# Performance work log

Measured on AMD Instinct MI355X. Metric: run time of the kernel, lower is better.

Reference implementation:

```python
import jax, jax.numpy as jnp
import numpy as np

N = 100000
E = 1600000
G = 128


def _degrees(src, dst, n):
    ones = jnp.ones(src.shape[0], dtype=jnp.float32)
    deg_out = jax.ops.segment_sum(ones, src, num_segments=n)
    deg_in = jax.ops.segment_sum(ones, dst, num_segments=n)
    return jnp.maximum(deg_out, 1.0), jnp.maximum(deg_in, 1.0)


def gcn_conv(x, W, b, src, dst, norm_out, norm_in):
    # DGL GraphConv, norm='both': scale src by d_out^-1/2, sum over edges,
    # scale dst by d_in^-1/2, then linear. Weight applied first (out<=in) --
    # mathematically identical, cheaper gather.
    h = (x * norm_out[:, None]) @ W          # [N, out]
    m = h[src]                               # [E, out] gather
    agg = jax.ops.segment_sum(m, dst, num_segments=N)  # [N, out] scatter-add
    return agg * norm_in[:, None] + b


def setup_inputs() -> dict:
    key = jax.random.key(0)
    ks = jax.random.split(key, 8)
    x = jax.random.normal(ks[0], (N, 128), dtype=jnp.float32)
    W1 = jax.random.normal(ks[1], (128, 64), dtype=jnp.float32) * (1.0 / np.sqrt(128))
    b1 = jnp.zeros((64,), dtype=jnp.float32)
    W2 = jax.random.normal(ks[2], (64, 16), dtype=jnp.float32) * (1.0 / np.sqrt(64))
    b2 = jnp.zeros((16,), dtype=jnp.float32)
    src = jax.random.randint(ks[3], (E,), 0, N, dtype=jnp.int32)
    dst = jax.random.randint(ks[4], (E,), 0, N, dtype=jnp.int32)
    graph_ids = jnp.sort(jax.random.randint(ks[5], (N,), 0, G, dtype=jnp.int32))
    return {"x": x, "W1": W1, "b1": b1, "W2": W2, "b2": b2,
            "src": src, "dst": dst, "graph_ids": graph_ids}


def reference(x, W1, b1, W2, b2, src, dst, graph_ids):
    deg_out, deg_in = _degrees(src, dst, N)
    norm_out = jax.lax.rsqrt(deg_out)
    norm_in = jax.lax.rsqrt(deg_in)
    h = gcn_conv(x, W1, b1, src, dst, norm_out, norm_in)
    h = jax.nn.relu(h)
    # dropout(p=0.2) is identity in eval mode
    h = gcn_conv(h, W2, b2, src, dst, norm_out, norm_in)
    # dgl.mean_nodes: per-graph mean pooling
    sums = jax.ops.segment_sum(h, graph_ids, num_segments=G)      # [G, 16]
    counts = jax.ops.segment_sum(jnp.ones((N,), jnp.float32), graph_ids, num_segments=G)
    return sums / jnp.maximum(counts, 1.0)[:, None]
```

## Files before the change

kernel.cpp:

```cpp
#include <hip/hip_runtime.h>
#include <hip/hip_fp16.h>

#define N_NODES 100000
#define N_EDGES 1600000
#define N_GRAPHS 128
#define SB 391
#define CAP 4608
#define NBLK 512
#define NE4 (N_EDGES / 4)
#define CH4 782
#define LDX 136

typedef unsigned long long u64;
typedef unsigned int u32;
typedef unsigned char u8;
typedef _Float16 f16;
typedef f16 half8 __attribute__((ext_vector_type(8)));
typedef f16 half4v __attribute__((ext_vector_type(4)));
typedef float floatx4 __attribute__((ext_vector_type(4)));

__global__ void k_init(int* __restrict__ cur_d, int* __restrict__ cur_s) {
  int t = blockIdx.x * blockDim.x + threadIdx.x;
  if (t < SB) { cur_d[t] = t * CAP; cur_s[t] = t * CAP; }
}

__global__ __launch_bounds__(256) void k_fuse(const int4* __restrict__ src4,
                                              const int4* __restrict__ dst4,
                                              int* __restrict__ cur_d,
                                              int* __restrict__ cur_s,
                                              u32* __restrict__ ed,
                                              u8* __restrict__ ssk8) {
  __shared__ int hd[SB], hs[SB], ld[SB], ls[SB];
  const int t = threadIdx.x, b = blockIdx.x;
  for (int j = t; j < SB; j += 256) { hd[j] = 0; hs[j] = 0; }
  __syncthreads();
  const int start = b * CH4, end = min(start + CH4, NE4);
  for (int i = start + t; i < end; i += 256) {
    int4 d = dst4[i]; int4 s = src4[i];
    atomicAdd(&hd[d.x >> 8], 1); atomicAdd(&hd[d.y >> 8], 1);
    atomicAdd(&hd[d.z >> 8], 1); atomicAdd(&hd[d.w >> 8], 1);
    atomicAdd(&hs[s.x >> 8], 1); atomicAdd(&hs[s.y >> 8], 1);
    atomicAdd(&hs[s.z >> 8], 1); atomicAdd(&hs[s.w >> 8], 1);
  }
  __syncthreads();
  for (int j = t; j < SB; j += 256) {
    ld[j] = atomicAdd(&cur_d[j], hd[j]);
    ls[j] = atomicAdd(&cur_s[j], hs[j]);
  }
  __syncthreads();
  for (int i = start + t; i < end; i += 256) {
    int4 d4 = dst4[i]; int4 s4 = src4[i];
    {
      int d = d4.x, s = s4.x;
      int pd = atomicAdd(&ld[d >> 8], 1);
      ed[pd] = ((u32)(d & 255) << 24) | (u32)s;
      int ps = atomicAdd(&ls[s >> 8], 1);
      ssk8[ps] = (u8)(s & 255);
    }
    {
      int d = d4.y, s = s4.y;
      int pd = atomicAdd(&ld[d >> 8], 1);
      ed[pd] = ((u32)(d & 255) << 24) | (u32)s;
      int ps = atomicAdd(&ls[s >> 8], 1);
      ssk8[ps] = (u8)(s & 255);
    }
    {
      int d = d4.z, s = s4.z;
      int pd = atomicAdd(&ld[d >> 8], 1);
      ed[pd] = ((u32)(d & 255) << 24) | (u32)s;
      int ps = atomicAdd(&ls[s >> 8], 1);
      ssk8[ps] = (u8)(s & 255);
    }
    {
      int d = d4.w, s = s4.w;
      int pd = atomicAdd(&ld[d >> 8], 1);
      ed[pd] = ((u32)(d & 255) << 24) | (u32)s;
      int ps = atomicAdd(&ls[s >> 8], 1);
      ssk8[ps] = (u8)(s & 255);
    }
  }
}

__global__ __launch_bounds__(256) void k_bucket_csr(const u32* __restrict__ ed,
                                                    const u8* __restrict__ ssk8,
                                                    const int* __restrict__ cur_d,
                                                    const int* __restrict__ cur_s,
                                                    int* __restrict__ row_ptr,
                                                    int* __restrict__ deg,
                                                    float* __restrict__ norm_in,
                                                    float* __restrict__ norm_out,
                                                    int* __restrict__ edge_src) {
  __shared__ int hist[256], scanbuf[256], cursor[256], hist2[256];
  const int b = blockIdx.x, t = threadIdx.x;
  const int base = b << 8;
  const int lo = b * CAP;
  const int hiD = cur_d[b];
  const int hiS = cur_s[b];
  hist[t] = 0; hist2[t] = 0;
  __syncthreads();
  for (int i = lo + t; i < hiS; i += 256) atomicAdd(&hist2[ssk8[i]], 1);
  for (int i = lo + t; i < hiD; i += 256) atomicAdd(&hist[ed[i] >> 24], 1);
  __syncthreads();
  int node = base + t;
  if (node < N_NODES)
    norm_out[node] = rsqrtf(fmaxf((float)hist2[t], 1.0f));
  int v = hist[t];
  scanbuf[t] = v;
  __syncthreads();
  for (int off = 1; off < 256; off <<= 1) {
    int a = (t >= off) ? scanbuf[t - off] : 0;
    __syncthreads(); scanbuf[t] += a; __syncthreads();
  }
  int excl = scanbuf[t] - v;
  if (node < N_NODES) {
    row_ptr[node] = lo + excl;
    deg[node] = v;
    norm_in[node] = rsqrtf(fmaxf((float)v, 1.0f));
  }
  cursor[t] = excl;
  __syncthreads();
  for (int i = lo + t; i < hiD; i += 256) {
    u32 e = ed[i];
    int p = atomicAdd(&cursor[e >> 24], 1);
    edge_src[lo + p] = (int)(e & 0x00FFFFFFu);
  }
}

__global__ __launch_bounds__(256) void k_gemm1(const float* __restrict__ x,
                                               const float* __restrict__ W1,
                                               const float* __restrict__ norm_out,
                                               __half* __restrict__ h1h) {
  __shared__ __align__(16) f16 Xs[64 * LDX];
  __shared__ __align__(16) f16 Ws[64 * LDX];
  const int t = threadIdx.x;
  const int row0 = blockIdx.x * 64;

  const float4* W4 = (const float4*)W1;
  for (int i = t; i < 2048; i += 256) {
    int k = i >> 4, n4 = (i & 15) * 4;
    float4 v = W4[i];
    Ws[(n4 + 0) * LDX + k] = (f16)v.x;
    Ws[(n4 + 1) * LDX + k] = (f16)v.y;
    Ws[(n4 + 2) * LDX + k] = (f16)v.z;
    Ws[(n4 + 3) * LDX + k] = (f16)v.w;
  }
  const float4* x4 = (const float4*)x;
  #pragma unroll
  for (int i = 0; i < 8; ++i) {
    int idx = t + 256 * i;
    int r = idx >> 5, c4 = idx & 31;
    int row = row0 + r;
    float4 v = make_float4(0.f, 0.f, 0.f, 0.f);
    if (row < N_NODES) {
      float s = norm_out[row];
      v = x4[(size_t)row * 32 + c4];
      v.x *= s; v.y *= s; v.z *= s; v.w *= s;
    }
    half4v h = { (f16)v.x, (f16)v.y, (f16)v.z, (f16)v.w };
    *(half4v*)&Xs[r * LDX + c4 * 4] = h;
  }
  __syncthreads();

  const int w = t >> 6, l = t & 63;
  const int m = l & 15, quad = l >> 4;
  floatx4 c0 = {0.f,0.f,0.f,0.f}, c1 = {0.f,0.f,0.f,0.f};
  floatx4 c2 = {0.f,0.f,0.f,0.f}, c3 = {0.f,0.f,0.f,0.f};
  const f16* xrow = &Xs[(w * 16 + m) * LDX + quad * 8];
  const f16* wrow = &Ws[m * LDX + quad * 8];
  #pragma unroll
  for (int kb = 0; kb < 4; ++kb) {
    half8 a  = *(const half8*)(xrow + kb * 32);
    half8 b0 = *(const half8*)(wrow + kb * 32);
    half8 b1 = *(const half8*)(wrow + 16 * LDX + kb * 32);
    half8 b2 = *(const half8*)(wrow + 32 * LDX + kb * 32);
    half8 b3 = *(const half8*)(wrow + 48 * LDX + kb * 32);
    c0 = __builtin_amdgcn_mfma_f32_16x16x32_f16(a, b0, c0, 0, 0, 0);
    c1 = __builtin_amdgcn_mfma_f32_16x16x32_f16(a, b1, c1, 0, 0, 0);
    c2 = __builtin_amdgcn_mfma_f32_16x16x32_f16(a, b2, c2, 0, 0, 0);
    c3 = __builtin_amdgcn_mfma_f32_16x16x32_f16(a, b3, c3, 0, 0, 0);
  }
  #pragma unroll
  for (int r = 0; r < 4; ++r) {
    int row = row0 + w * 16 + quad * 4 + r;
    if (row < N_NODES + 1) {
      __half* dst = h1h + (size_t)row * 64 + m;
      dst[0]  = __float2half(c0[r]);
      dst[16] = __float2half(c1[r]);
      dst[32] = __float2half(c2[r]);
      dst[48] = __float2half(c3[r]);
    }
  }
}

__global__ __launch_bounds__(256) void k_gather_l1(const int* __restrict__ row_ptr,
                                                   const int* __restrict__ deg,
                                                   const int* __restrict__ edge_src,
                                                   const __half* __restrict__ h1h,
                                                   const float* __restrict__ norm_in,
                                                   const float* __restrict__ norm_out,
                                                   const float* __restrict__ b1,
                                                   const float* __restrict__ W2,
                                                   __half* __restrict__ h2h) {
  __shared__ __align__(16) f16 Ws2[16 * 72];
  __shared__ __align__(16) f16 Rs[4][16 * 72];
  const int t = threadIdx.x;
  for (int i = t; i < 1024; i += 256) {
    int k = i >> 4, n = i & 15;
    Ws2[n * 72 + k] = (f16)W2[i];
  }
  if (blockIdx.x == 0 && t < 16) h2h[(size_t)N_NODES * 16 + t] = __float2half(0.f);
  __syncthreads();

  const int w = t >> 6, l = t & 63;
  const int base = blockIdx.x * 64 + w * 16;
  if (base >= N_NODES) return;

  const int m = l & 15, q4 = l >> 4;
  const int node_l = min(base + m, N_NODES - 1);
  const int my_lo = row_ptr[node_l];
  const u32 my_deg = (u32)deg[node_l];
  const int lo_blk = __shfl(my_lo, 0, 64);
  const int hi_blk = __shfl(my_lo + (int)my_deg, 15, 64);

  const int s1e = 8 * (m >> 2) + (m & 3);
  const int s2e = s1e + 4;

  union U4 { u32 u[4]; half8 h; uint4 v; };

  U4 ib0, ib1;
  #pragma unroll
  for (int wj = 0; wj < 4; ++wj) {
    int k0 = q4 * 8 + 2 * wj, k1 = k0 + 1;
    ib0.u[wj] = (k0 == m      ? 0x3C00u : 0u) | (k1 == m      ? 0x3C000000u : 0u);
    ib1.u[wj] = (k0 == m + 16 ? 0x3C00u : 0u) | (k1 == m + 16 ? 0x3C000000u : 0u);
  }

  const uint4* __restrict__ h1u4 = (const uint4*)h1h;
  floatx4 acc0 = {0.f,0.f,0.f,0.f}, acc1 = {0.f,0.f,0.f,0.f};
  floatx4 acc2 = {0.f,0.f,0.f,0.f}, acc3 = {0.f,0.f,0.f,0.f};
  const floatx4 zf = {0.f,0.f,0.f,0.f};

  uint4 pa0, pa1, pb0, pb1;
  #define LOADC(CB) do {                                                      \
    int i1 = (CB) + s1e, i2 = (CB) + s2e;                                     \
    int sv1 = (i1 < hi_blk) ? edge_src[i1] : (int)N_NODES;                    \
    int sv2 = (i2 < hi_blk) ? edge_src[i2] : (int)N_NODES;                    \
    size_t r1 = (size_t)(u32)sv1 * 8u, r2 = (size_t)(u32)sv2 * 8u;            \
    pa0 = h1u4[r1 + (u32)q4];       pa1 = h1u4[r1 + 4u + (u32)q4];            \
    pb0 = h1u4[r2 + (u32)q4];       pb1 = h1u4[r2 + 4u + (u32)q4];            \
  } while (0)

  if (lo_blk < hi_blk) LOADC(lo_blk);
  #pragma unroll 1
  for (int cb = lo_blk; cb < hi_blk; cb += 32) {
    U4 ca0, ca1, cbb0, cbb1;
    ca0.v = pa0; ca1.v = pa1; cbb0.v = pb0; cbb1.v = pb1;
    if (cb + 32 < hi_blk) LOADC(cb + 32);

    u32 e0 = (u32)(cb - my_lo) + (u32)(q4 * 8);
    U4 s;
    s.u[0] = ((e0+0u)<my_deg?0x3C00u:0u) | ((e0+1u)<my_deg?0x3C000000u:0u);
    s.u[1] = ((e0+2u)<my_deg?0x3C00u:0u) | ((e0+3u)<my_deg?0x3C000000u:0u);
    s.u[2] = ((e0+4u)<my_deg?0x3C00u:0u) | ((e0+5u)<my_deg?0x3C000000u:0u);
    s.u[3] = ((e0+6u)<my_deg?0x3C00u:0u) | ((e0+7u)<my_deg?0x3C000000u:0u);

    {
      floatx4 o10 = __builtin_amdgcn_mfma_f32_16x16x32_f16(ca0.h,  ib0.h, zf, 0, 0, 0);
      floatx4 o11 = __builtin_amdgcn_mfma_f32_16x16x32_f16(ca0.h,  ib1.h, zf, 0, 0, 0);
      floatx4 o20 = __builtin_amdgcn_mfma_f32_16x16x32_f16(cbb0.h, ib0.h, zf, 0, 0, 0);
      floatx4 o21 = __builtin_amdgcn_mfma_f32_16x16x32_f16(cbb0.h, ib1.h, zf, 0, 0, 0);
      half8 bf0 = { (f16)o10[0], (f16)o10[1], (f16)o10[2], (f16)o10[3],
                    (f16)o20[0], (f16)o20[1], (f16)o20[2], (f16)o20[3] };
      half8 bf1 = { (f16)o11[0], (f16)o11[1], (f16)o11[2], (f16)o11[3],
                    (f16)o21[0], (f16)o21[1], (f16)o21[2], (f16)o21[3] };
      acc0 = __builtin_amdgcn_mfma_f32_16x16x32_f16(s.h, bf0, acc0, 0, 0, 0);
      acc1 = __builtin_amdgcn_mfma_f32_16x16x32_f16(s.h, bf1, acc1, 0, 0, 0);
    }
    {
      floatx4 o10 = __builtin_amdgcn_mfma_f32_16x16x32_f16(ca1.h,  ib0.h, zf, 0, 0, 0);
      floatx4 o11 = __builtin_amdgcn_mfma_f32_16x16x32_f16(ca1.h,  ib1.h, zf, 0, 0, 0);
      floatx4 o20 = __builtin_amdgcn_mfma_f32_16x16x32_f16(cbb1.h, ib0.h, zf, 0, 0, 0);
      floatx4 o21 = __builtin_amdgcn_mfma_f32_16x16x32_f16(cbb1.h, ib1.h, zf, 0, 0, 0);
      half8 bf0 = { (f16)o10[0], (f16)o10[1], (f16)o10[2], (f16)o10[3],
                    (f16)o20[0], (f16)o20[1], (f16)o20[2], (f16)o20[3] };
      half8 bf1 = { (f16)o11[0], (f16)o11[1], (f16)o11[2], (f16)o11[3],
                    (f16)o21[0], (f16)o21[1], (f16)o21[2], (f16)o21[3] };
      acc2 = __builtin_amdgcn_mfma_f32_16x16x32_f16(s.h, bf0, acc2, 0, 0, 0);
      acc3 = __builtin_amdgcn_mfma_f32_16x16x32_f16(s.h, bf1, acc3, 0, 0, 0);
    }
  }
  #undef LOADC

  const float bg0 = b1[m], bg1 = b1[16 + m], bg2 = b1[32 + m], bg3 = b1[48 + m];
  f16* Rw = &Rs[w][0];
  #pragma unroll
  for (int r = 0; r < 4; ++r) {
    int row = base + q4 * 4 + r;
    float ni = (row < N_NODES) ? norm_in[row] : 0.f;
    f16* dst = &Rw[(q4 * 4 + r) * 72 + m];
    dst[0]  = (f16)fmaxf(acc0[r] * ni + bg0, 0.f);
    dst[16] = (f16)fmaxf(acc1[r] * ni + bg1, 0.f);
    dst[32] = (f16)fmaxf(acc2[r] * ni + bg2, 0.f);
    dst[48] = (f16)fmaxf(acc3[r] * ni + bg3, 0.f);
  }
  asm volatile("s_waitcnt lgkmcnt(0)" ::: "memory");
  __builtin_amdgcn_sched_barrier(0);

  const f16* ra = &Rw[m * 72 + q4 * 8];
  const f16* rb = &Ws2[m * 72 + q4 * 8];
  half8 a0 = *(const half8*)ra;
  half8 a1 = *(const half8*)(ra + 32);
  half8 wb0 = *(const half8*)rb;
  half8 wb1 = *(const half8*)(rb + 32);
  floatx4 cc = {0.f,0.f,0.f,0.f};
  cc = __builtin_amdgcn_mfma_f32_16x16x32_f16(a0, wb0, cc, 0, 0, 0);
  cc = __builtin_amdgcn_mfma_f32_16x16x32_f16(a1, wb1, cc, 0, 0, 0);
  #pragma unroll
  for (int r = 0; r < 4; ++r) {
    int row = base + q4 * 4 + r;
    if (row < N_NODES)
      h2h[(size_t)row * 16 + m] = __float2half(cc[r] * norm_out[row]);
  }
}

__global__ __launch_bounds__(256) void k_gather_l2(const int* __restrict__ row_ptr,
                                                   const int* __restrict__ deg,
                                                   const int* __restrict__ edge_src,
                                                   const __half* __restrict__ h2h,
                                                   const float* __restrict__ norm_in,
                                                   float* __restrict__ agg2) {
  const int t = threadIdx.x;
  const int w = t >> 6;
  const int l = t & 63;
  const int n = blockIdx.x * 4 + w;
  const int f2 = l & 7;
  const int p = l >> 3;

  const u32* __restrict__ h2u = (const u32*)h2h;
  const int lo = row_ptr[n], hi = lo + deg[n];

  float ax = 0.f, ay = 0.f, bx = 0.f, by = 0.f;
  for (int base = lo; base < hi; base += 16) {
    int i1 = base + p, i2 = base + p + 8;
    int s0 = (i1 < hi) ? edge_src[i1] : (int)N_NODES;
    int s1 = (i2 < hi) ? edge_src[i2] : (int)N_NODES;
    u32 v0 = h2u[(u32)s0 * 8u + (u32)f2];
    u32 v1 = h2u[(u32)s1 * 8u + (u32)f2];
    float2 g0 = __half22float2(*(__half2*)&v0);
    float2 g1 = __half22float2(*(__half2*)&v1);
    ax += g0.x; ay += g0.y;
    bx += g1.x; by += g1.y;
  }
  float sx = ax + bx, sy = ay + by;
  sx += __shfl_xor(sx, 8, 64);  sy += __shfl_xor(sy, 8, 64);
  sx += __shfl_xor(sx, 16, 64); sy += __shfl_xor(sy, 16, 64);
  sx += __shfl_xor(sx, 32, 64); sy += __shfl_xor(sy, 32, 64);
  if (l < 8) {
    float ni = norm_in[n];
    ((float2*)agg2)[(size_t)n * 8 + f2] = make_float2(sx * ni, sy * ni);
  }
}

__global__ __launch_bounds__(256) void k_pool(const float* __restrict__ agg2,
                                              const float* __restrict__ b2,
                                              const int* __restrict__ gid,
                                              float* __restrict__ out) {
  const int g = blockIdx.x;
  __shared__ int s_lo, s_hi;
  if (threadIdx.x == 0) {
    int a = 0, b = N_NODES;
    while (a < b) { int m = (a + b) >> 1; if (gid[m] < g) a = m + 1; else b = m; }
    s_lo = a;
    b = N_NODES;
    while (a < b) { int m = (a + b) >> 1; if (gid[m] < g + 1) a = m + 1; else b = m; }
    s_hi = a;
  }
  __syncthreads();
  const int lo = s_lo, hi = s_hi, cnt = hi - lo;
  const int j = threadIdx.x & 15;
  const int r = threadIdx.x >> 4;
  float acc = 0.f;
  for (int n = lo + r; n < hi; n += 16)
    acc += agg2[(size_t)n * 16 + j];

  __shared__ float red[256];
  red[threadIdx.x] = acc;
  __syncthreads();
  #pragma unroll
  for (int s = 8; s > 0; s >>= 1) {
    if (r < s) red[threadIdx.x] += red[threadIdx.x + s * 16];
    __syncthreads();
  }
  if (r == 0)
    out[g * 16 + j] = (cnt > 0) ? (red[j] / (float)cnt + b2[j]) : 0.0f;
}

extern "C" void kernel_launch(void* const* d_in, const int* in_sizes, int n_in,
                              void* d_out, int out_size, void* d_ws, size_t ws_size,
                              hipStream_t stream) {
  const float* x   = (const float*)d_in[0];
  const float* W1  = (const float*)d_in[1];
  const float* b1  = (const float*)d_in[2];
  const float* W2  = (const float*)d_in[3];
  const float* b2  = (const float*)d_in[4];
  const int*   src = (const int*)d_in[5];
  const int*   dst = (const int*)d_in[6];
  const int*   gid = (const int*)d_in[7];
  float* out = (float*)d_out;

  int* wsi = (int*)d_ws;
  float* wsf = (float*)d_ws;

  float* norm_out = wsf + 0;
  float* norm_in  = wsf + 100000;
  int*   row_ptr  = wsi + 200000;
  int*   deg      = wsi + 300000;
  int*   cur_d    = wsi + 400000;
  int*   cur_s    = wsi + 400400;
  int*   edge_src = wsi + 400800;
  const size_t S  = 2202528;
  u8*    ssk8     = (u8*)(wsi + S);
  u32*   ed       = (u32*)(wsi + S + 450432);
  __half* h1h     = (__half*)(wsi + S);
  __half* h2h     = (__half*)(wsi + S + 3200032);
  float*  agg2    = (float*)(wsi + S);

  const int4* src4 = (const int4*)src;
  const int4* dst4 = (const int4*)dst;

  k_init      <<<2, 256, 0, stream>>>(cur_d, cur_s);
  k_fuse      <<<NBLK, 256, 0, stream>>>(src4, dst4, cur_d, cur_s, ed, ssk8);
  k_bucket_csr<<<SB, 256, 0, stream>>>(ed, ssk8, cur_d, cur_s, row_ptr, deg,
                                       norm_in, norm_out, edge_src);
  k_gemm1     <<<(N_NODES + 64) / 64, 256, 0, stream>>>(x, W1, norm_out, h1h);
  k_gather_l1 <<<(N_NODES + 63) / 64, 256, 0, stream>>>(row_ptr, deg, edge_src, h1h,
                                                        norm_in, norm_out, b1, W2, h2h);
  k_gather_l2 <<<N_NODES / 4, 256, 0, stream>>>(row_ptr, deg, edge_src, h2h,
                                                norm_in, agg2);
  k_pool      <<<N_GRAPHS, 256, 0, stream>>>(agg2, b2, gid, out);
}
```

Before: 267.4 us.

## Split layer-1 gather edge chunks across four waves per 16-node group

Each block now handles 16 nodes instead of 64, and its four waves take interleaved 32-edge chunks of that group's edge range rather than each wave owning its own 16 nodes. Partial MFMA accumulators from waves 1-3 are reduced through shared memory into wave 0, which then applies bias, ReLU and the second-layer GEMM. This shortens each wave's serial edge loop and raises memory-level parallelism. The cost is four times as many blocks, an extra shared-memory reduction and barrier, and three idle waves during the epilogue.

```diff
diff --git a/kernel.cpp b/kernel.cpp
--- a/kernel.cpp
+++ b/kernel.cpp
@@ -202,21 +202,19 @@
                                                    const float* __restrict__ W2,
                                                    __half* __restrict__ h2h) {
   __shared__ __align__(16) f16 Ws2[16 * 72];
-  __shared__ __align__(16) f16 Rs[4][16 * 72];
+  __shared__ __align__(16) f16 Rs[16 * 72];
+  __shared__ __align__(16) float redbuf[3][64][20];
   const int t = threadIdx.x;
   for (int i = t; i < 1024; i += 256) {
     int k = i >> 4, n = i & 15;
     Ws2[n * 72 + k] = (f16)W2[i];
   }
   if (blockIdx.x == 0 && t < 16) h2h[(size_t)N_NODES * 16 + t] = __float2half(0.f);
-  __syncthreads();
 
   const int w = t >> 6, l = t & 63;
-  const int base = blockIdx.x * 64 + w * 16;
-  if (base >= N_NODES) return;
-
+  const int base = blockIdx.x * 16;
   const int m = l & 15, q4 = l >> 4;
-  const int node_l = min(base + m, N_NODES - 1);
+  const int node_l = base + m;
   const int my_lo = row_ptr[node_l];
   const u32 my_deg = (u32)deg[node_l];
   const int lo_blk = __shfl(my_lo, 0, 64);
@@ -250,12 +248,13 @@
     pb0 = h1u4[r2 + (u32)q4];       pb1 = h1u4[r2 + 4u + (u32)q4];            \
   } while (0)
 
-  if (lo_blk < hi_blk) LOADC(lo_blk);
+  const int cb0 = lo_blk + w * 32;
+  if (cb0 < hi_blk) LOADC(cb0);
   #pragma unroll 1
-  for (int cb = lo_blk; cb < hi_blk; cb += 32) {
+  for (int cb = cb0; cb < hi_blk; cb += 128) {
     U4 ca0, ca1, cbb0, cbb1;
     ca0.v = pa0; ca1.v = pa1; cbb0.v = pb0; cbb1.v = pb1;
-    if (cb + 32 < hi_blk) LOADC(cb + 32);
+    if (cb + 128 < hi_blk) LOADC(cb + 128);
 
     u32 e0 = (u32)(cb - my_lo) + (u32)(q4 * 8);
     U4 s;
@@ -291,13 +290,24 @@
   }
   #undef LOADC
 
+  if (w > 0) {
+    floatx4* wp = (floatx4*)&redbuf[w - 1][l][0];
+    wp[0] = acc0; wp[1] = acc1; wp[2] = acc2; wp[3] = acc3;
+  }
+  __syncthreads();
+  if (w != 0) return;
+  #pragma unroll
+  for (int k = 0; k < 3; ++k) {
+    const floatx4* rp = (const floatx4*)&redbuf[k][l][0];
+    acc0 += rp[0]; acc1 += rp[1]; acc2 += rp[2]; acc3 += rp[3];
+  }
+
   const float bg0 = b1[m], bg1 = b1[16 + m], bg2 = b1[32 + m], bg3 = b1[48 + m];
-  f16* Rw = &Rs[w][0];
   #pragma unroll
   for (int r = 0; r < 4; ++r) {
     int row = base + q4 * 4 + r;
-    float ni = (row < N_NODES) ? norm_in[row] : 0.f;
-    f16* dst = &Rw[(q4 * 4 + r) * 72 + m];
+    float ni = norm_in[row];
+    f16* dst = &Rs[(q4 * 4 + r) * 72 + m];
     dst[0]  = (f16)fmaxf(acc0[r] * ni + bg0, 0.f);
     dst[16] = (f16)fmaxf(acc1[r] * ni + bg1, 0.f);
     dst[32] = (f16)fmaxf(acc2[r] * ni + bg2, 0.f);
@@ -306,7 +316,7 @@
   asm volatile("s_waitcnt lgkmcnt(0)" ::: "memory");
   __builtin_amdgcn_sched_barrier(0);
 
-  const f16* ra = &Rw[m * 72 + q4 * 8];
+  const f16* ra = &Rs[m * 72 + q4 * 8];
   const f16* rb = &Ws2[m * 72 + q4 * 8];
   half8 a0 = *(const half8*)ra;
   half8 a1 = *(const half8*)(ra + 32);
@@ -318,8 +328,7 @@
   #pragma unroll
   for (int r = 0; r < 4; ++r) {
     int row = base + q4 * 4 + r;
-    if (row < N_NODES)
-      h2h[(size_t)row * 16 + m] = __float2half(cc[r] * norm_out[row]);
+    h2h[(size_t)row * 16 + m] = __float2half(cc[r] * norm_out[row]);
   }
 }
 
@@ -433,8 +442,8 @@
   k_bucket_csr<<<SB, 256, 0, stream>>>(ed, ssk8, cur_d, cur_s, row_ptr, deg,
                                        norm_in, norm_out, edge_src);
   k_gemm1     <<<(N_NODES + 64) / 64, 256, 0, stream>>>(x, W1, norm_out, h1h);
-  k_gather_l1 <<<(N_NODES + 63) / 64, 256, 0, stream>>>(row_ptr, deg, edge_src, h1h,
-                                                        norm_in, norm_out, b1, W2, h2h);
+  k_gather_l1 <<<N_NODES / 16, 256, 0, stream>>>(row_ptr, deg, edge_src, h1h,
+                                                 norm_in, norm_out, b1, W2, h2h);
   k_gather_l2 <<<N_NODES / 4, 256, 0, stream>>>(row_ptr, deg, edge_src, h2h,
                                                 norm_in, agg2);
   k_pool      <<<N_GRAPHS, 256, 0, stream>>>(agg2, b2, gid, out);
```

After: 269.1 us. Within noise of the previous version (+0.6%).

## Partition each node's edges by source window for cache-local layer-1 gather

Applied to the files above, without the earlier changes.

During CSR construction, each node's incoming edges are reordered by which quarter of the source-node range they come from. The per-window offsets are packed into the upper bits of the degree word. The layer-1 gather then runs four passes per wave, one per source window, staging edge indices in LDS so that each pass gathers from a smaller slice of h1 that is more likely to stay in cache. The trade-offs are extra serial per-node loops in the bucket kernel, partially filled 32-edge chunks in every pass, a 512-entry per-wave index cap, and packed counts that assume degrees below 256.

```diff
diff --git a/kernel.cpp b/kernel.cpp
--- a/kernel.cpp
+++ b/kernel.cpp
@@ -10,6 +10,7 @@
 #define NE4 (N_EDGES / 4)
 #define CH4 782
 #define LDX 136
+#define NWIN 25000
 
 typedef unsigned long long u64;
 typedef unsigned int u32;
@@ -91,6 +92,7 @@
                                                     float* __restrict__ norm_out,
                                                     int* __restrict__ edge_src) {
   __shared__ int hist[256], scanbuf[256], cursor[256], hist2[256];
+  __shared__ int sbuf[CAP], sbuf2[CAP];
   const int b = blockIdx.x, t = threadIdx.x;
   const int base = b << 8;
   const int lo = b * CAP;
@@ -114,7 +116,6 @@
   int excl = scanbuf[t] - v;
   if (node < N_NODES) {
     row_ptr[node] = lo + excl;
-    deg[node] = v;
     norm_in[node] = rsqrtf(fmaxf((float)v, 1.0f));
   }
   cursor[t] = excl;
@@ -122,8 +123,29 @@
   for (int i = lo + t; i < hiD; i += 256) {
     u32 e = ed[i];
     int p = atomicAdd(&cursor[e >> 24], 1);
-    edge_src[lo + p] = (int)(e & 0x00FFFFFFu);
-  }
+    sbuf[p] = (int)(e & 0x00FFFFFFu);
+  }
+  __syncthreads();
+  int c0 = 0, c1 = 0, c2 = 0, c3 = 0;
+  for (int i = excl; i < excl + v; ++i) {
+    int s = sbuf[i]; int wd = s / NWIN;
+    c0 += (wd == 0); c1 += (wd == 1); c2 += (wd == 2); c3 += (wd == 3);
+  }
+  int k0 = excl, k1 = excl + c0, k2 = k1 + c1, k3 = k2 + c2;
+  for (int i = excl; i < excl + v; ++i) {
+    int s = sbuf[i]; int wd = s / NWIN;
+    int pos;
+    if (wd == 0)      pos = k0++;
+    else if (wd == 1) pos = k1++;
+    else if (wd == 2) pos = k2++;
+    else              pos = k3++;
+    sbuf2[pos] = s;
+  }
+  if (node < N_NODES)
+    deg[node] = v | (c0 << 8) | ((c0 + c1) << 16) | ((c0 + c1 + c2) << 24);
+  __syncthreads();
+  const int cnt = hiD - lo;
+  for (int i = t; i < cnt; i += 256) edge_src[lo + i] = sbuf2[i];
 }
 
 __global__ __launch_bounds__(256) void k_gemm1(const float* __restrict__ x,
@@ -192,17 +214,18 @@
   }
 }
 
-__global__ __launch_bounds__(256) void k_gather_l1(const int* __restrict__ row_ptr,
-                                                   const int* __restrict__ deg,
-                                                   const int* __restrict__ edge_src,
-                                                   const __half* __restrict__ h1h,
-                                                   const float* __restrict__ norm_in,
-                                                   const float* __restrict__ norm_out,
-                                                   const float* __restrict__ b1,
-                                                   const float* __restrict__ W2,
-                                                   __half* __restrict__ h2h) {
+__global__ __launch_bounds__(256, 6) void k_gather_l1(const int* __restrict__ row_ptr,
+                                                      const int* __restrict__ deg,
+                                                      const int* __restrict__ edge_src,
+                                                      const __half* __restrict__ h1h,
+                                                      const float* __restrict__ norm_in,
+                                                      const float* __restrict__ norm_out,
+                                                      const float* __restrict__ b1,
+                                                      const float* __restrict__ W2,
+                                                      __half* __restrict__ h2h) {
   __shared__ __align__(16) f16 Ws2[16 * 72];
   __shared__ __align__(16) f16 Rs[4][16 * 72];
+  __shared__ int Eidx[4][512];
   const int t = threadIdx.x;
   for (int i = t; i < 1024; i += 256) {
     int k = i >> 4, n = i & 15;
@@ -216,11 +239,11 @@
   if (base >= N_NODES) return;
 
   const int m = l & 15, q4 = l >> 4;
-  const int node_l = min(base + m, N_NODES - 1);
+  const int node_l = base + m;
   const int my_lo = row_ptr[node_l];
-  const u32 my_deg = (u32)deg[node_l];
-  const int lo_blk = __shfl(my_lo, 0, 64);
-  const int hi_blk = __shfl(my_lo + (int)my_deg, 15, 64);
+  const int dw = deg[node_l];
+  const int dgr = dw & 255;
+  const int a1 = (dw >> 8) & 255, a2 = (dw >> 16) & 255, a3 = (dw >> 24) & 255;
 
   const int s1e = 8 * (m >> 2) + (m & 3);
   const int s2e = s1e + 4;
@@ -241,54 +264,80 @@
   const floatx4 zf = {0.f,0.f,0.f,0.f};
 
   uint4 pa0, pa1, pb0, pb1;
-  #define LOADC(CB) do {                                                      \
-    int i1 = (CB) + s1e, i2 = (CB) + s2e;                                     \
-    int sv1 = (i1 < hi_blk) ? edge_src[i1] : (int)N_NODES;                    \
-    int sv2 = (i2 < hi_blk) ? edge_src[i2] : (int)N_NODES;                    \
+  #define LOADC(C, T) do {                                                    \
+    int p1i = 32 * (C) + s1e, p2i = 32 * (C) + s2e;                           \
+    int sv1 = (p1i < (T)) ? Eidx[w][p1i] : (int)N_NODES;                      \
+    int sv2 = (p2i < (T)) ? Eidx[w][p2i] : (int)N_NODES;                      \
     size_t r1 = (size_t)(u32)sv1 * 8u, r2 = (size_t)(u32)sv2 * 8u;            \
     pa0 = h1u4[r1 + (u32)q4];       pa1 = h1u4[r1 + 4u + (u32)q4];            \
     pb0 = h1u4[r2 + (u32)q4];       pb1 = h1u4[r2 + 4u + (u32)q4];            \
   } while (0)
 
-  if (lo_blk < hi_blk) LOADC(lo_blk);
-  #pragma unroll 1
-  for (int cb = lo_blk; cb < hi_blk; cb += 32) {
-    U4 ca0, ca1, cbb0, cbb1;
-    ca0.v = pa0; ca1.v = pa1; cbb0.v = pb0; cbb1.v = pb1;
-    if (cb + 32 < hi_blk) LOADC(cb + 32);
-
-    u32 e0 = (u32)(cb - my_lo) + (u32)(q4 * 8);
-    U4 s;
-    s.u[0] = ((e0+0u)<my_deg?0x3C00u:0u) | ((e0+1u)<my_deg?0x3C000000u:0u);
-    s.u[1] = ((e0+2u)<my_deg?0x3C00u:0u) | ((e0+3u)<my_deg?0x3C000000u:0u);
-    s.u[2] = ((e0+4u)<my_deg?0x3C00u:0u) | ((e0+5u)<my_deg?0x3C000000u:0u);
-    s.u[3] = ((e0+6u)<my_deg?0x3C00u:0u) | ((e0+7u)<my_deg?0x3C000000u:0u);
-
-    {
-      floatx4 o10 = __builtin_amdgcn_mfma_f32_16x16x32_f16(ca0.h,  ib0.h, zf, 0, 0, 0);
-      floatx4 o11 = __builtin_amdgcn_mfma_f32_16x16x32_f16(ca0.h,  ib1.h, zf, 0, 0, 0);
-      floatx4 o20 = __builtin_amdgcn_mfma_f32_16x16x32_f16(cbb0.h, ib0.h, zf, 0, 0, 0);
-      floatx4 o21 = __builtin_amdgcn_mfma_f32_16x16x32_f16(cbb0.h, ib1.h, zf, 0, 0, 0);
-      half8 bf0 = { (f16)o10[0], (f16)o10[1], (f16)o10[2], (f16)o10[3],
-                    (f16)o20[0], (f16)o20[1], (f16)o20[2], (f16)o20[3] };
-      half8 bf1 = { (f16)o11[0], (f16)o11[1], (f16)o11[2], (f16)o11[3],
-                    (f16)o21[0], (f16)o21[1], (f16)o21[2], (f16)o21[3] };
-      acc0 = __builtin_amdgcn_mfma_f32_16x16x32_f16(s.h, bf0, acc0, 0, 0, 0);
-      acc1 = __builtin_amdgcn_mfma_f32_16x16x32_f16(s.h, bf1, acc1, 0, 0, 0);
-    }
-    {
-      floatx4 o10 = __builtin_amdgcn_mfma_f32_16x16x32_f16(ca1.h,  ib0.h, zf, 0, 0, 0);
-      floatx4 o11 = __builtin_amdgcn_mfma_f32_16x16x32_f16(ca1.h,  ib1.h, zf, 0, 0, 0);
-      floatx4 o20 = __builtin_amdgcn_mfma_f32_16x16x32_f16(cbb1.h, ib0.h, zf, 0, 0, 0);
-      floatx4 o21 = __builtin_amdgcn_mfma_f32_16x16x32_f16(cbb1.h, ib1.h, zf, 0, 0, 0);
-      half8 bf0 = { (f16)o10[0], (f16)o10[1], (f16)o10[2], (f16)o10[3],
-                    (f16)o20[0], (f16)o20[1], (f16)o20[2], (f16)o20[3] };
-      half8 bf1 = { (f16)o11[0], (f16)o11[1], (f16)o11[2], (f16)o11[3],
-                    (f16)o21[0], (f16)o21[1], (f16)o21[2], (f16)o21[3] };
-      acc2 = __builtin_amdgcn_mfma_f32_16x16x32_f16(s.h, bf0, acc2, 0, 0, 0);
-      acc3 = __builtin_amdgcn_mfma_f32_16x16x32_f16(s.h, bf1, acc3, 0, 0, 0);
-    }
-  }
+  #define PASS(AP, AP1) do {                                                  \
+    const int cntw = (AP1) - (AP);                                            \
+    int Pi = cntw;                                                            \
+    _Pragma("unroll")                                                         \
+    for (int sft = 1; sft < 16; sft <<= 1) {                                  \
+      int tv = __shfl(Pi, (l & 48) | ((m - sft) & 15), 64);                   \
+      if (m >= sft) Pi += tv;                                                 \
+    }                                                                         \
+    const int Pex = Pi - cntw;                                                \
+    int T = __shfl(Pi, (l & 48) | 15, 64);                                    \
+    if (T > 512) T = 512;                                                     \
+    if (q4 == 0) {                                                            \
+      int gs = my_lo + (AP);                                                  \
+      for (int i = 0; i < cntw && (Pex + i) < 512; ++i)                       \
+        Eidx[w][Pex + i] = edge_src[gs + i];                                  \
+    }                                                                         \
+    asm volatile("s_waitcnt lgkmcnt(0)" ::: "memory");                        \
+    __builtin_amdgcn_sched_barrier(0);                                        \
+    const int nc = (T + 31) >> 5;                                             \
+    if (nc > 0) {                                                             \
+      LOADC(0, T);                                                            \
+      _Pragma("unroll 1")                                                     \
+      for (int c = 0; c < nc; ++c) {                                          \
+        U4 ca0, ca1, cbb0, cbb1;                                              \
+        ca0.v = pa0; ca1.v = pa1; cbb0.v = pb0; cbb1.v = pb1;                 \
+        if (c + 1 < nc) LOADC(c + 1, T);                                      \
+        u32 e0 = (u32)(32 * c - Pex) + (u32)(q4 * 8);                         \
+        U4 s;                                                                 \
+        s.u[0] = ((e0+0u)<(u32)cntw?0x3C00u:0u) | ((e0+1u)<(u32)cntw?0x3C000000u:0u); \
+        s.u[1] = ((e0+2u)<(u32)cntw?0x3C00u:0u) | ((e0+3u)<(u32)cntw?0x3C000000u:0u); \
+        s.u[2] = ((e0+4u)<(u32)cntw?0x3C00u:0u) | ((e0+5u)<(u32)cntw?0x3C000000u:0u); \
+        s.u[3] = ((e0+6u)<(u32)cntw?0x3C00u:0u) | ((e0+7u)<(u32)cntw?0x3C000000u:0u); \
+        {                                                                     \
+          floatx4 o10 = __builtin_amdgcn_mfma_f32_16x16x32_f16(ca0.h,  ib0.h, zf, 0, 0, 0); \
+          floatx4 o11 = __builtin_amdgcn_mfma_f32_16x16x32_f16(ca0.h,  ib1.h, zf, 0, 0, 0); \
+          floatx4 o20 = __builtin_amdgcn_mfma_f32_16x16x32_f16(cbb0.h, ib0.h, zf, 0, 0, 0); \
+          floatx4 o21 = __builtin_amdgcn_mfma_f32_16x16x32_f16(cbb0.h, ib1.h, zf, 0, 0, 0); \
+          half8 bf0 = { (f16)o10[0], (f16)o10[1], (f16)o10[2], (f16)o10[3],   \
+                        (f16)o20[0], (f16)o20[1], (f16)o20[2], (f16)o20[3] }; \
+          half8 bf1 = { (f16)o11[0], (f16)o11[1], (f16)o11[2], (f16)o11[3],   \
+                        (f16)o21[0], (f16)o21[1], (f16)o21[2], (f16)o21[3] }; \
+          acc0 = __builtin_amdgcn_mfma_f32_16x16x32_f16(s.h, bf0, acc0, 0, 0, 0); \
+          acc1 = __builtin_amdgcn_mfma_f32_16x16x32_f16(s.h, bf1, acc1, 0, 0, 0); \
+        }                                                                     \
+        {                                                                     \
+          floatx4 o10 = __builtin_amdgcn_mfma_f32_16x16x32_f16(ca1.h,  ib0.h, zf, 0, 0, 0); \
+          floatx4 o11 = __builtin_amdgcn_mfma_f32_16x16x32_f16(ca1.h,  ib1.h, zf, 0, 0, 0); \
+          floatx4 o20 = __builtin_amdgcn_mfma_f32_16x16x32_f16(cbb1.h, ib0.h, zf, 0, 0, 0); \
+          floatx4 o21 = __builtin_amdgcn_mfma_f32_16x16x32_f16(cbb1.h, ib1.h, zf, 0, 0, 0); \
+          half8 bf0 = { (f16)o10[0], (f16)o10[1], (f16)o10[2], (f16)o10[3],   \
+                        (f16)o20[0], (f16)o20[1], (f16)o20[2], (f16)o20[3] }; \
+          half8 bf1 = { (f16)o11[0], (f16)o11[1], (f16)o11[2], (f16)o11[3],   \
+                        (f16)o21[0], (f16)o21[1], (f16)o21[2], (f16)o21[3] }; \
+          acc2 = __builtin_amdgcn_mfma_f32_16x16x32_f16(s.h, bf0, acc2, 0, 0, 0); \
+          acc3 = __builtin_amdgcn_mfma_f32_16x16x32_f16(s.h, bf1, acc3, 0, 0, 0); \
+        }                                                                     \
+      }                                                                       \
+    }                                                                         \
+  } while (0)
+
+  PASS(0, a1);
+  PASS(a1, a2);
+  PASS(a2, a3);
+  PASS(a3, dgr);
+  #undef PASS
   #undef LOADC
 
   const float bg0 = b1[m], bg1 = b1[16 + m], bg2 = b1[32 + m], bg3 = b1[48 + m];
@@ -296,7 +345,7 @@
   #pragma unroll
   for (int r = 0; r < 4; ++r) {
     int row = base + q4 * 4 + r;
-    float ni = (row < N_NODES) ? norm_in[row] : 0.f;
+    float ni = norm_in[row];
     f16* dst = &Rw[(q4 * 4 + r) * 72 + m];
     dst[0]  = (f16)fmaxf(acc0[r] * ni + bg0, 0.f);
     dst[16] = (f16)fmaxf(acc1[r] * ni + bg1, 0.f);
@@ -309,17 +358,16 @@
   const f16* ra = &Rw[m * 72 + q4 * 8];
   const f16* rb = &Ws2[m * 72 + q4 * 8];
   half8 a0 = *(const half8*)ra;
-  half8 a1 = *(const half8*)(ra + 32);
+  half8 a1v = *(const half8*)(ra + 32);
   half8 wb0 = *(const half8*)rb;
   half8 wb1 = *(const half8*)(rb + 32);
   floatx4 cc = {0.f,0.f,0.f,0.f};
   cc = __builtin_amdgcn_mfma_f32_16x16x32_f16(a0, wb0, cc, 0, 0, 0);
-  cc = __builtin_amdgcn_mfma_f32_16x16x32_f16(a1, wb1, cc, 0, 0, 0);
+  cc = __builtin_amdgcn_mfma_f32_16x16x32_f16(a1v, wb1, cc, 0, 0, 0);
   #pragma unroll
   for (int r = 0; r < 4; ++r) {
     int row = base + q4 * 4 + r;
-    if (row < N_NODES)
-      h2h[(size_t)row * 16 + m] = __float2half(cc[r] * norm_out[row]);
+    h2h[(size_t)row * 16 + m] = __float2half(cc[r] * norm_out[row]);
   }
 }
 
@@ -337,7 +385,7 @@
   const int p = l >> 3;
 
   const u32* __restrict__ h2u = (const u32*)h2h;
-  const int lo = row_ptr[n], hi = lo + deg[n];
+  const int lo = row_ptr[n], hi = lo + (deg[n] & 255);
 
   float ax = 0.f, ay = 0.f, bx = 0.f, by = 0.f;
   for (int base = lo; base < hi; base += 16) {
```

New measurement: 296.2 us. 10.8% more time.

## Stage bucketed edges in shared memory before coalesced scatter to global

Applied to the files above, without the earlier changes.

The fused bucketing kernel now loads each thread's edge chunk into registers once, instead of reading src/dst twice. It prefix-scans the per-block histograms and sorts edges into shared-memory buffers by bucket, then writes them out so that consecutive threads hit contiguous global addresses within each bucket. This replaces scattered 4-byte and 1-byte global stores. The cost is extra shared memory (about 19KB, which may lower occupancy), two block scans with many barriers, and a second pass over shared memory.

```diff
diff --git a/kernel.cpp b/kernel.cpp
--- a/kernel.cpp
+++ b/kernel.cpp
@@ -9,10 +9,12 @@
 #define NBLK 512
 #define NE4 (N_EDGES / 4)
 #define CH4 782
+#define CMAX 3200
 #define LDX 136
 
 typedef unsigned long long u64;
 typedef unsigned int u32;
+typedef unsigned short u16;
 typedef unsigned char u8;
 typedef _Float16 f16;
 typedef f16 half8 __attribute__((ext_vector_type(8)));
@@ -31,53 +33,114 @@
                                               u32* __restrict__ ed,
                                               u8* __restrict__ ssk8) {
   __shared__ int hd[SB], hs[SB], ld[SB], ls[SB];
+  __shared__ int lofsD[SB], lofsS[SB], curD[SB], curS[SB];
+  __shared__ int S[512];
+  __shared__ u32 edbuf[CMAX];
+  __shared__ u16 bidD[CMAX], bidS[CMAX];
+  __shared__ u8  ssbuf[CMAX];
   const int t = threadIdx.x, b = blockIdx.x;
   for (int j = t; j < SB; j += 256) { hd[j] = 0; hs[j] = 0; }
   __syncthreads();
   const int start = b * CH4, end = min(start + CH4, NE4);
-  for (int i = start + t; i < end; i += 256) {
-    int4 d = dst4[i]; int4 s = src4[i];
-    atomicAdd(&hd[d.x >> 8], 1); atomicAdd(&hd[d.y >> 8], 1);
-    atomicAdd(&hd[d.z >> 8], 1); atomicAdd(&hd[d.w >> 8], 1);
-    atomicAdd(&hs[s.x >> 8], 1); atomicAdd(&hs[s.y >> 8], 1);
-    atomicAdd(&hs[s.z >> 8], 1); atomicAdd(&hs[s.w >> 8], 1);
-  }
-  __syncthreads();
+  const int nit = end - start;
+
+  int4 sv[4], dv[4];
+  int nh = 0;
+  #pragma unroll
+  for (int k = 0; k < 4; ++k) {
+    int i = start + t + 256 * k;
+    if (i < nit + start) { sv[k] = src4[i]; dv[k] = dst4[i]; nh = k + 1; }
+  }
+
+  #pragma unroll
+  for (int k = 0; k < 4; ++k) {
+    if (k < nh) {
+      int4 d = dv[k]; int4 s = sv[k];
+      atomicAdd(&hd[d.x >> 8], 1); atomicAdd(&hd[d.y >> 8], 1);
+      atomicAdd(&hd[d.z >> 8], 1); atomicAdd(&hd[d.w >> 8], 1);
+      atomicAdd(&hs[s.x >> 8], 1); atomicAdd(&hs[s.y >> 8], 1);
+      atomicAdd(&hs[s.z >> 8], 1); atomicAdd(&hs[s.w >> 8], 1);
+    }
+  }
+  __syncthreads();
+
   for (int j = t; j < SB; j += 256) {
     ld[j] = atomicAdd(&cur_d[j], hd[j]);
     ls[j] = atomicAdd(&cur_s[j], hs[j]);
   }
-  __syncthreads();
-  for (int i = start + t; i < end; i += 256) {
-    int4 d4 = dst4[i]; int4 s4 = src4[i];
-    {
-      int d = d4.x, s = s4.x;
-      int pd = atomicAdd(&ld[d >> 8], 1);
-      ed[pd] = ((u32)(d & 255) << 24) | (u32)s;
-      int ps = atomicAdd(&ls[s >> 8], 1);
-      ssk8[ps] = (u8)(s & 255);
+
+  S[t] = (t < SB) ? hd[t] : 0;
+  S[t + 256] = (t + 256 < SB) ? hd[t + 256] : 0;
+  __syncthreads();
+  for (int off = 1; off < 512; off <<= 1) {
+    int a0 = (t >= off) ? S[t - off] : 0;
+    int a1 = (t + 256 >= off) ? S[t + 256 - off] : 0;
+    __syncthreads();
+    S[t] += a0; S[t + 256] += a1;
+    __syncthreads();
+  }
+  if (t < SB) { lofsD[t] = S[t] - hd[t]; curD[t] = S[t] - hd[t]; }
+  if (t + 256 < SB) { lofsD[t + 256] = S[t + 256] - hd[t + 256]; curD[t + 256] = S[t + 256] - hd[t + 256]; }
+  __syncthreads();
+
+  S[t] = (t < SB) ? hs[t] : 0;
+  S[t + 256] = (t + 256 < SB) ? hs[t + 256] : 0;
+  __syncthreads();
+  for (int off = 1; off < 512; off <<= 1) {
+    int a0 = (t >= off) ? S[t - off] : 0;
+    int a1 = (t + 256 >= off) ? S[t + 256 - off] : 0;
+    __syncthreads();
+    S[t] += a0; S[t + 256] += a1;
+    __syncthreads();
+  }
+  if (t < SB) { lofsS[t] = S[t] - hs[t]; curS[t] = S[t] - hs[t]; }
+  if (t + 256 < SB) { lofsS[t + 256] = S[t + 256] - hs[t + 256]; curS[t + 256] = S[t + 256] - hs[t + 256]; }
+  __syncthreads();
+
+  #pragma unroll
+  for (int k = 0; k < 4; ++k) {
+    if (k < nh) {
+      int4 d4 = dv[k]; int4 s4 = sv[k];
+      {
+        int d = d4.x, s = s4.x; int j = d >> 8;
+        int p = atomicAdd(&curD[j], 1);
+        edbuf[p] = ((u32)(d & 255) << 24) | (u32)s; bidD[p] = (u16)j;
+        int js = s >> 8; int ps = atomicAdd(&curS[js], 1);
+        ssbuf[ps] = (u8)(s & 255); bidS[ps] = (u16)js;
+      }
+      {
+        int d = d4.y, s = s4.y; int j = d >> 8;
+        int p = atomicAdd(&curD[j], 1);
+        edbuf[p] = ((u32)(d & 255) << 24) | (u32)s; bidD[p] = (u16)j;
+        int js = s >> 8; int ps = atomicAdd(&curS[js], 1);
+        ssbuf[ps] = (u8)(s & 255); bidS[ps] = (u16)js;
+      }
+      {
+        int d = d4.z, s = s4.z; int j = d >> 8;
+        int p = atomicAdd(&curD[j], 1);
+        edbuf[p] = ((u32)(d & 255) << 24) | (u32)s; bidD[p] = (u16)j;
+        int js = s >> 8; int ps = atomicAdd(&curS[js], 1);
+        ssbuf[ps] = (u8)(s & 255); bidS[ps] = (u16)js;
+      }
+      {
+        int d = d4.w, s = s4.w; int j = d >> 8;
+        int p = atomicAdd(&curD[j], 1);
+        edbuf[p] = ((u32)(d & 255) << 24) | (u32)s; bidD[p] = (u16)j;
+        int js = s >> 8; int ps = atomicAdd(&curS[js], 1);
+        ssbuf[ps] = (u8)(s & 255); bidS[ps] = (u16)js;
+      }
     }
-    {
-      int d = d4.y, s = s4.y;
-      int pd = atomicAdd(&ld[d >> 8], 1);
-      ed[pd] = ((u32)(d & 255) << 24) | (u32)s;
-      int ps = atomicAdd(&ls[s >> 8], 1);
-      ssk8[ps] = (u8)(s & 255);
-    }
-    {
-      int d = d4.z, s = s4.z;
-      int pd = atomicAdd(&ld[d >> 8], 1);
-      ed[pd] = ((u32)(d & 255) << 24) | (u32)s;
-      int ps = atomicAdd(&ls[s >> 8], 1);
-      ssk8[ps] = (u8)(s & 255);
-    }
-    {
-      int d = d4.w, s = s4.w;
-      int pd = atomicAdd(&ld[d >> 8], 1);
-      ed[pd] = ((u32)(d & 255) << 24) | (u32)s;
-      int ps = atomicAdd(&ls[s >> 8], 1);
-      ssk8[ps] = (u8)(s & 255);
-    }
+  }
+  __syncthreads();
+
+  const int cnt = nit * 4;
+  for (int i = t; i < cnt; i += 256) {
+    int j = bidD[i];
+    ed[ld[j] + i - lofsD[j]] = edbuf[i];
+  }
+  for (int i = t; i < cnt; i += 256) {
+    int j = bidS[i];
+    ssk8[ls[j] + i - lofsS[j]] = ssbuf[i];
   }
 }
 
```

New measurement: 258.1 us. 3.5% less time.
